# Optimization experiments

Measured on AMD Instinct MI355X. Metric: run time of the kernel, lower is better.

The kernel has to match this reference:

```python
import jax, jax.numpy as jnp
import numpy as np

N, K, D = 8192, 512, 4096

def setup_inputs() -> dict:
    key = jax.random.key(0)
    k1, k2, k3 = jax.random.split(key, 3)
    features = jax.random.normal(k1, (N, K), dtype=jnp.float32)
    w = jax.random.normal(k2, (D, N), dtype=jnp.float32)
    E = jax.random.normal(k3, (K, D), dtype=jnp.float32) / np.sqrt(K)  # embed_matrix (k x d)
    b = jnp.zeros((D,), dtype=jnp.float32)  # bias initialized to zeros in the module
    return {"features": features, "w": w, "E": E, "b": b}

def reference(features, w, E, b):
    # Linear: y = features @ E + b  -> (N, D)   (torch weight is E.mT, so x @ W.T == x @ E)
    y = features @ E + b
    # diag(y @ w): equivalent to row-wise dot products, same math without the NxN matmul
    return jnp.einsum("nd,dn->n", y, w)
```

## Files before the change

### kernel.cpp

```cpp
#include <hip/hip_runtime.h>

#define N_DIM 8192
#define K_DIM 512
#define D_DIM 4096

typedef __bf16 bf16x8 __attribute__((ext_vector_type(8)));
typedef float  f32x16 __attribute__((ext_vector_type(16)));
typedef unsigned short u16x8 __attribute__((ext_vector_type(8)));

__device__ __forceinline__ unsigned short f2bf(float f) {
    union { float f; unsigned int u; } v; v.f = f;
    unsigned int r = v.u + 0x7FFF + ((v.u >> 16) & 1);
    return (unsigned short)(r >> 16);
}

__global__ __launch_bounds__(256) void transpose_E(const float* __restrict__ E,
                                                   unsigned short* __restrict__ ET) {
    __shared__ float tile[64][65];
    const int d0 = blockIdx.x * 64;
    const int k0 = blockIdx.y * 64;
    const int tid = threadIdx.x;
    const int r  = tid / 16;
    const int c4 = (tid % 16) * 4;
#pragma unroll
    for (int p = 0; p < 4; ++p) {
        int k = p * 16 + r;
        float4 v = *reinterpret_cast<const float4*>(E + (size_t)(k0 + k) * D_DIM + d0 + c4);
        tile[k][c4 + 0] = v.x; tile[k][c4 + 1] = v.y;
        tile[k][c4 + 2] = v.z; tile[k][c4 + 3] = v.w;
    }
    __syncthreads();
#pragma unroll
    for (int p = 0; p < 4; ++p) {
        int d = p * 16 + r;
        ushort4 o;
        o.x = f2bf(tile[c4 + 0][d]);
        o.y = f2bf(tile[c4 + 1][d]);
        o.z = f2bf(tile[c4 + 2][d]);
        o.w = f2bf(tile[c4 + 3][d]);
        *reinterpret_cast<ushort4*>(ET + (size_t)(d0 + d) * K_DIM + k0 + c4) = o;
    }
}

__global__ __launch_bounds__(256) void convert_F(const float* __restrict__ F,
                                                 unsigned short* __restrict__ FB) {
    const int idx8 = (blockIdx.x * 256 + threadIdx.x) * 8;
    float4 a = *reinterpret_cast<const float4*>(F + idx8);
    float4 b = *reinterpret_cast<const float4*>(F + idx8 + 4);
    u16x8 o;
    o[0] = f2bf(a.x); o[1] = f2bf(a.y); o[2] = f2bf(a.z); o[3] = f2bf(a.w);
    o[4] = f2bf(b.x); o[5] = f2bf(b.y); o[6] = f2bf(b.z); o[7] = f2bf(b.w);
    *reinterpret_cast<u16x8*>(FB + idx8) = o;
}

__global__ __launch_bounds__(256) void gemm_fused(const unsigned short* __restrict__ FB,
                                                  const float* __restrict__ W,
                                                  const unsigned short* __restrict__ ET,
                                                  const float* __restrict__ B,
                                                  float* __restrict__ out) {
    __shared__ unsigned short Ash[2 * 128 * 32];
    __shared__ unsigned short Bsh[2 * 128 * 32];

    const int tid  = threadIdx.x;
    const int wave = tid >> 6;
    const int lane = tid & 63;
    const int wy   = wave >> 1;
    const int wx   = wave & 1;
    const int l31  = lane & 31;
    const int half = lane >> 5;

    const int d0 = blockIdx.y * 128;
    const int n0 = blockIdx.x * 128;

    f32x16 acc[2][2] = {};

    const int srow   = lane >> 2;
    const int schunk = (((lane & 3) ^ ((srow >> 1) & 3)) * 8);

    for (int kt = 0; kt < K_DIM / 64; ++kt) {
        const int kb = kt * 64;
#pragma unroll
        for (int p = 0; p < 2; ++p) {
#pragma unroll
            for (int jj = 0; jj < 2; ++jj) {
                const int j = wave * 2 + jj;
                const unsigned short* ga =
                    ET + (size_t)(d0 + j * 16 + srow) * K_DIM + kb + p * 32 + schunk;
                __builtin_amdgcn_global_load_lds(
                    (const __attribute__((address_space(1))) void*)ga,
                    (__attribute__((address_space(3))) void*)(Ash + p * 4096 + j * 512),
                    16, 0, 0);
                const unsigned short* gb =
                    FB + (size_t)(n0 + j * 16 + srow) * K_DIM + kb + p * 32 + schunk;
                __builtin_amdgcn_global_load_lds(
                    (const __attribute__((address_space(1))) void*)gb,
                    (__attribute__((address_space(3))) void*)(Bsh + p * 4096 + j * 512),
                    16, 0, 0);
            }
        }
        __syncthreads();

#pragma unroll
        for (int ks = 0; ks < 4; ++ks) {
            const int p = ks >> 1;
            const int c = (ks & 1) * 2 + half;
            bf16x8 af[2], bf[2];
#pragma unroll
            for (int mi = 0; mi < 2; ++mi) {
                const int R = wy * 64 + mi * 32 + l31;
                const int slot = c ^ ((R >> 1) & 3);
                af[mi] = *reinterpret_cast<const bf16x8*>(
                    Ash + p * 4096 + R * 32 + slot * 8);
            }
#pragma unroll
            for (int ni = 0; ni < 2; ++ni) {
                const int R = wx * 64 + ni * 32 + l31;
                const int slot = c ^ ((R >> 1) & 3);
                bf[ni] = *reinterpret_cast<const bf16x8*>(
                    Bsh + p * 4096 + R * 32 + slot * 8);
            }
#pragma unroll
            for (int mi = 0; mi < 2; ++mi)
#pragma unroll
                for (int ni = 0; ni < 2; ++ni)
                    acc[mi][ni] = __builtin_amdgcn_mfma_f32_32x32x16_bf16(
                        af[mi], bf[ni], acc[mi][ni], 0, 0, 0);
        }
        __syncthreads();
    }

    const int nb = n0 + wx * 64;
    float part0 = 0.f, part1 = 0.f;
#pragma unroll
    for (int mi = 0; mi < 2; ++mi) {
        const int dbase = d0 + wy * 64 + mi * 32 + 4 * half;
#pragma unroll
        for (int reg = 0; reg < 16; ++reg) {
            const int dd = dbase + (reg & 3) + 8 * (reg >> 2);
            const float bd = B[dd];
            const float* wr = W + (size_t)dd * N_DIM + nb;
            part0 += (acc[mi][0][reg] + bd) * wr[l31];
            part1 += (acc[mi][1][reg] + bd) * wr[32 + l31];
        }
    }
    part0 += __shfl_xor(part0, 32);
    part1 += __shfl_xor(part1, 32);
    if (lane < 32) {
        atomicAdd(out + nb + l31, part0);
        atomicAdd(out + nb + 32 + l31, part1);
    }
}

extern "C" void kernel_launch(void* const* d_in, const int* in_sizes, int n_in,
                              void* d_out, int out_size, void* d_ws, size_t ws_size,
                              hipStream_t stream) {
    const float* F = (const float*)d_in[0];
    const float* W = (const float*)d_in[1];
    const float* E = (const float*)d_in[2];
    const float* B = (const float*)d_in[3];
    float* out = (float*)d_out;

    unsigned short* ET = (unsigned short*)d_ws;
    unsigned short* FB = (unsigned short*)((char*)d_ws + (size_t)D_DIM * K_DIM * 2);

    hipMemsetAsync(d_out, 0, (size_t)out_size * sizeof(float), stream);
    transpose_E<<<dim3(D_DIM / 64, K_DIM / 64), 256, 0, stream>>>(E, ET);
    convert_F<<<dim3(N_DIM * K_DIM / (256 * 8)), 256, 0, stream>>>(F, FB);
    gemm_fused<<<dim3(N_DIM / 128, D_DIM / 128), 256, 0, stream>>>(FB, W, ET, B, out);
}
```

Baseline: 241.5 us.

## Widen GEMM tile to 128x256 with XCD-aware block remapping

Doubles the N extent of each block's tile to 256, so each wave computes 2x4 MFMA tiles instead of 2x2, which halves the number of blocks and the redundant reloads of ET. The 1D grid is remapped so that blocks landing on the same XCD share N and D tiles, aiming for better L2 reuse. W loads in the epilogue become nontemporal, and launch bounds request 2 blocks per SM. The larger accumulator array raises register pressure, and there are fewer blocks to spread across CUs.

Measured after the change: 249.7 us. 3.4% more time.

```diff
diff --git a/kernel.cpp b/kernel.cpp
--- a/kernel.cpp
+++ b/kernel.cpp
@@ -53,13 +53,13 @@
     *reinterpret_cast<u16x8*>(FB + idx8) = o;
 }
 
-__global__ __launch_bounds__(256) void gemm_fused(const unsigned short* __restrict__ FB,
-                                                  const float* __restrict__ W,
-                                                  const unsigned short* __restrict__ ET,
-                                                  const float* __restrict__ B,
-                                                  float* __restrict__ out) {
+__global__ __launch_bounds__(256, 2) void gemm_fused(const unsigned short* __restrict__ FB,
+                                                     const float* __restrict__ W,
+                                                     const unsigned short* __restrict__ ET,
+                                                     const float* __restrict__ B,
+                                                     float* __restrict__ out) {
     __shared__ unsigned short Ash[2 * 128 * 32];
-    __shared__ unsigned short Bsh[2 * 128 * 32];
+    __shared__ unsigned short Bsh[2 * 256 * 32];
 
     const int tid  = threadIdx.x;
     const int wave = tid >> 6;
@@ -69,10 +69,15 @@
     const int l31  = lane & 31;
     const int half = lane >> 5;
 
-    const int d0 = blockIdx.y * 128;
-    const int n0 = blockIdx.x * 128;
+    const int f     = blockIdx.x;
+    const int xcd   = f & 7;
+    const int s     = f >> 3;
+    const int ntile = (xcd & 3) * 8 + (s & 7);
+    const int dtile = (xcd >> 2) * 16 + (s >> 3);
+    const int n0 = ntile * 256;
+    const int d0 = dtile * 128;
 
-    f32x16 acc[2][2] = {};
+    f32x16 acc[2][4] = {};
 
     const int srow   = lane >> 2;
     const int schunk = (((lane & 3) ^ ((srow >> 1) & 3)) * 8);
@@ -90,11 +95,15 @@
                     (const __attribute__((address_space(1))) void*)ga,
                     (__attribute__((address_space(3))) void*)(Ash + p * 4096 + j * 512),
                     16, 0, 0);
+            }
+#pragma unroll
+            for (int jj = 0; jj < 4; ++jj) {
+                const int j = wave * 4 + jj;
                 const unsigned short* gb =
                     FB + (size_t)(n0 + j * 16 + srow) * K_DIM + kb + p * 32 + schunk;
                 __builtin_amdgcn_global_load_lds(
                     (const __attribute__((address_space(1))) void*)gb,
-                    (__attribute__((address_space(3))) void*)(Bsh + p * 4096 + j * 512),
+                    (__attribute__((address_space(3))) void*)(Bsh + p * 8192 + j * 512),
                     16, 0, 0);
             }
         }
@@ -104,7 +113,7 @@
         for (int ks = 0; ks < 4; ++ks) {
             const int p = ks >> 1;
             const int c = (ks & 1) * 2 + half;
-            bf16x8 af[2], bf[2];
+            bf16x8 af[2], bf[4];
 #pragma unroll
             for (int mi = 0; mi < 2; ++mi) {
                 const int R = wy * 64 + mi * 32 + l31;
@@ -113,24 +122,24 @@
                     Ash + p * 4096 + R * 32 + slot * 8);
             }
 #pragma unroll
-            for (int ni = 0; ni < 2; ++ni) {
-                const int R = wx * 64 + ni * 32 + l31;
+            for (int ni = 0; ni < 4; ++ni) {
+                const int R = wx * 128 + ni * 32 + l31;
                 const int slot = c ^ ((R >> 1) & 3);
                 bf[ni] = *reinterpret_cast<const bf16x8*>(
-                    Bsh + p * 4096 + R * 32 + slot * 8);
+                    Bsh + p * 8192 + R * 32 + slot * 8);
             }
 #pragma unroll
             for (int mi = 0; mi < 2; ++mi)
 #pragma unroll
-                for (int ni = 0; ni < 2; ++ni)
+                for (int ni = 0; ni < 4; ++ni)
                     acc[mi][ni] = __builtin_amdgcn_mfma_f32_32x32x16_bf16(
                         af[mi], bf[ni], acc[mi][ni], 0, 0, 0);
         }
         __syncthreads();
     }
 
-    const int nb = n0 + wx * 64;
-    float part0 = 0.f, part1 = 0.f;
+    const int nb = n0 + wx * 128;
+    float part[4] = {0.f, 0.f, 0.f, 0.f};
 #pragma unroll
     for (int mi = 0; mi < 2; ++mi) {
         const int dbase = d0 + wy * 64 + mi * 32 + 4 * half;
@@ -139,15 +148,17 @@
             const int dd = dbase + (reg & 3) + 8 * (reg >> 2);
             const float bd = B[dd];
             const float* wr = W + (size_t)dd * N_DIM + nb;
-            part0 += (acc[mi][0][reg] + bd) * wr[l31];
-            part1 += (acc[mi][1][reg] + bd) * wr[32 + l31];
+#pragma unroll
+            for (int ni = 0; ni < 4; ++ni)
+                part[ni] += (acc[mi][ni][reg] + bd) *
+                            __builtin_nontemporal_load(wr + ni * 32 + l31);
         }
     }
-    part0 += __shfl_xor(part0, 32);
-    part1 += __shfl_xor(part1, 32);
-    if (lane < 32) {
-        atomicAdd(out + nb + l31, part0);
-        atomicAdd(out + nb + 32 + l31, part1);
+#pragma unroll
+    for (int ni = 0; ni < 4; ++ni) {
+        part[ni] += __shfl_xor(part[ni], 32);
+        if (lane < 32)
+            atomicAdd(out + nb + ni * 32 + l31, part[ni]);
     }
 }
 
@@ -166,5 +177,5 @@
     hipMemsetAsync(d_out, 0, (size_t)out_size * sizeof(float), stream);
     transpose_E<<<dim3(D_DIM / 64, K_DIM / 64), 256, 0, stream>>>(E, ET);
     convert_F<<<dim3(N_DIM * K_DIM / (256 * 8)), 256, 0, stream>>>(F, FB);
-    gemm_fused<<<dim3(N_DIM / 128, D_DIM / 128), 256, 0, stream>>>(FB, W, ET, B, out);
+    gemm_fused<<<dim3((N_DIM / 256) * (D_DIM / 128)), 256, 0, stream>>>(FB, W, ET, B, out);
 }
```
